# Kernel tuning notes

Measured on AMD Instinct MI355X. Metric: run time of the kernel, lower is better.

## Reference

```python
import jax, jax.numpy as jnp
import numpy as np

NUM_NODES = 50000
NUM_EDGES = 800000
NUM_GRAPHS = 1024
D_IN = 64
D_PROT = 1280
HID = 256
OUT = 1


def setup_inputs() -> dict:
    key = jax.random.key(0)
    ks = jax.random.split(key, 16)
    s = 0.02
    x = jax.random.normal(ks[0], (NUM_NODES, D_IN), dtype=jnp.float32)
    edge_index = jax.random.randint(ks[1], (2, NUM_EDGES), 0, NUM_NODES, dtype=jnp.int32)
    batch = jnp.sort(jax.random.randint(ks[2], (NUM_NODES,), 0, NUM_GRAPHS, dtype=jnp.int32))
    protein_embedding = jax.random.normal(ks[3], (NUM_GRAPHS, D_PROT), dtype=jnp.float32)
    # SAGEConv params: lin_l (aggregated neighbors, with bias), lin_r (self, no bias)
    Wl = jax.random.normal(ks[4], (D_IN, HID), dtype=jnp.float32) * s
    bl = jnp.zeros((HID,), dtype=jnp.float32)
    Wr = jax.random.normal(ks[5], (D_IN, HID), dtype=jnp.float32) * s
    Wp = jax.random.normal(ks[6], (D_PROT, HID), dtype=jnp.float32) * s
    bp = jnp.zeros((HID,), dtype=jnp.float32)
    Wi = jax.random.normal(ks[7], (2 * HID, HID), dtype=jnp.float32) * s
    bi = jnp.zeros((HID,), dtype=jnp.float32)
    Wo = jax.random.normal(ks[8], (HID, OUT), dtype=jnp.float32) * s
    bo = jnp.zeros((OUT,), dtype=jnp.float32)
    return {"x": x, "protein_embedding": protein_embedding, "Wl": Wl, "bl": bl,
            "Wr": Wr, "Wp": Wp, "bp": bp, "Wi": Wi, "bi": bi, "Wo": Wo, "bo": bo,
            "edge_index": edge_index, "batch": batch}


def _segment_mean(vals, seg_ids, num_segments):
    sums = jax.ops.segment_sum(vals, seg_ids, num_segments=num_segments)
    cnt = jax.ops.segment_sum(jnp.ones((vals.shape[0],), vals.dtype), seg_ids,
                              num_segments=num_segments)
    return sums / jnp.maximum(cnt, 1.0)[:, None]


def reference(x, protein_embedding, Wl, bl, Wr, Wp, bp, Wi, bi, Wo, bo, edge_index, batch):
    src, dst = edge_index[0], edge_index[1]
    # SAGEConv: mean-aggregate neighbor messages at target nodes, then fuse linears
    aggr = _segment_mean(x[src], dst, NUM_NODES)           # [N, D_IN]
    drug_x = jax.nn.relu(aggr @ Wl + bl + x @ Wr)          # [N, HID]
    # global_mean_pool over graphs in the batch
    pooled = _segment_mean(drug_x, batch, NUM_GRAPHS)      # [G, HID]
    protein_x = protein_embedding @ Wp + bp                # [G, HID]
    combined = jnp.concatenate((pooled, protein_x), axis=1)  # [G, 2*HID]
    interaction = jax.nn.relu(combined @ Wi + bi)          # [G, HID]
    return interaction @ Wo + bo                           # [G, OUT]
```

## Files before the change

### kernel.cpp

```cpp
#include <hip/hip_runtime.h>
#include <hip/hip_bf16.h>

#define N_NODES 50000
#define N_EDGES 800000
#define N_GRAPHS 1024
#define D_IN 64
#define D_PROT 1280
#define HID 256
#define N_PAD 50048

#define NB 782
#define BCAP 2048
#define BEPB 4096
#define BBLK 196

typedef __attribute__((ext_vector_type(8))) short short8;
typedef __attribute__((ext_vector_type(4))) float f32x4;
typedef __hip_bfloat16 bf16;

__device__ inline unsigned bf16rne(float f) {
  unsigned u = __float_as_uint(f);
  return (u + 0x7fffu + ((u >> 16) & 1u)) >> 16;
}
__device__ inline void acc_bf2(float4& a, uint2 v) {
  a.x += __uint_as_float(v.x << 16);
  a.y += __uint_as_float(v.x & 0xffff0000u);
  a.z += __uint_as_float(v.y << 16);
  a.w += __uint_as_float(v.y & 0xffff0000u);
}

#define PREP_XC 3125
#define PREP_PE (PREP_XC + 1280)
#define PREP_PL (PREP_PE + 8)
#define PREP_PR (PREP_PL + 8)
#define PREP_WP (PREP_PR + 160)
#define PREP_WI (PREP_WP + 64)

__device__ inline void pack_frag(const float* __restrict__ src, bf16* __restrict__ dst,
                                 int KC, int tid) {
  int lane = tid & 63;
  int chunk = tid >> 6;
  int c = chunk / KC, kc = chunk - c * KC;
  int kbase = kc * 32 + ((lane >> 4) * 8);
  int n = c * 16 + (lane & 15);
#pragma unroll
  for (int j = 0; j < 8; ++j)
    dst[(size_t)tid * 8 + j] = __float2bfloat16(src[(size_t)(kbase + j) * HID + n]);
}

__global__ __launch_bounds__(256) void k_front(
    const float* __restrict__ x, const float* __restrict__ pe,
    const float* __restrict__ Wl, const float* __restrict__ Wr,
    const float* __restrict__ Wp, const float* __restrict__ Wi,
    const int* __restrict__ ei,
    uint2* __restrict__ x2, uint2* __restrict__ pe2,
    bf16* __restrict__ Wl_pk, bf16* __restrict__ Wr_pk,
    bf16* __restrict__ Wp_pk, bf16* __restrict__ Wi_pk,
    int* __restrict__ bcnt, unsigned* __restrict__ bped) {
  __shared__ int hist[NB];
  __shared__ int base[NB];
  const int b = blockIdx.x;
  const int t = threadIdx.x;
  if (b < BBLK) {
    const int e0 = b * BEPB;
    for (int i = t; i < NB; i += 256) hist[i] = 0;
    __syncthreads();
    for (int i = t; i < BEPB; i += 1024) {
      int d[4]; bool v[4];
#pragma unroll
      for (int u = 0; u < 4; ++u) {
        int idx = i + u * 256;
        v[u] = (e0 + idx < N_EDGES);
        d[u] = v[u] ? ei[N_EDGES + e0 + idx] : 0;
      }
#pragma unroll
      for (int u = 0; u < 4; ++u)
        if (v[u]) atomicAdd(&hist[d[u] >> 6], 1);
    }
    __syncthreads();
    for (int i = t; i < NB; i += 256) {
      int c = hist[i];
      base[i] = (c > 0) ? atomicAdd(&bcnt[i], c) : 0;
      hist[i] = 0;
    }
    __syncthreads();
    for (int i = t; i < BEPB; i += 1024) {
      int s[4], d[4]; bool v[4];
#pragma unroll
      for (int u = 0; u < 4; ++u) {
        int idx = i + u * 256;
        v[u] = (e0 + idx < N_EDGES);
        s[u] = v[u] ? ei[e0 + idx] : 0;
        d[u] = v[u] ? ei[N_EDGES + e0 + idx] : 0;
      }
#pragma unroll
      for (int u = 0; u < 4; ++u) {
        if (v[u]) {
          int bk = d[u] >> 6;
          int pos = base[bk] + atomicAdd(&hist[bk], 1);
          if (pos < BCAP)
            bped[(size_t)bk * BCAP + pos] =
                (unsigned)s[u] | ((unsigned)(d[u] & 63) << 16);
        }
      }
    }
    return;
  }
  const int pb = b - BBLK;
  if (pb < PREP_XC) {
    int tid = pb * 256 + t;
    float4 v = ((const float4*)x)[tid];
    x2[tid] = make_uint2(bf16rne(v.x) | (bf16rne(v.y) << 16),
                         bf16rne(v.z) | (bf16rne(v.w) << 16));
  } else if (pb < PREP_PE) {
    int tid = (pb - PREP_XC) * 256 + t;
    float4 v = ((const float4*)pe)[tid];
    pe2[tid] = make_uint2(bf16rne(v.x) | (bf16rne(v.y) << 16),
                          bf16rne(v.z) | (bf16rne(v.w) << 16));
  } else if (pb < PREP_PL) {
    pack_frag(Wl, Wl_pk, 2, (pb - PREP_PE) * 256 + t);
  } else if (pb < PREP_PR) {
    pack_frag(Wr, Wr_pk, 2, (pb - PREP_PL) * 256 + t);
  } else if (pb < PREP_WP) {
    pack_frag(Wp, Wp_pk, 40, (pb - PREP_PR) * 256 + t);
  } else {
    pack_frag(Wi, Wi_pk, 16, (pb - PREP_WP) * 256 + t);
  }
}

__global__ __launch_bounds__(256, 4) void k_mid(
    const uint2* __restrict__ x2, const unsigned* __restrict__ bped,
    const int* __restrict__ bcnt, const int* __restrict__ batch,
    const bf16* __restrict__ Wl_pk, const bf16* __restrict__ Wr_pk,
    const float* __restrict__ bl, float* __restrict__ poolsum,
    const bf16* __restrict__ pebf, const bf16* __restrict__ Wp_pk,
    float* __restrict__ prot4) {
  __shared__ unsigned s_raw[2304];
  __shared__ unsigned short s_e[BCAP];
  __shared__ int s_off[65];
  __shared__ int s_cur[64];
  __shared__ int s_batch[64];
  const int t = threadIdx.x;
  if (blockIdx.x < NB) {
    uint2* aggT = (uint2*)s_raw;
    const int b = blockIdx.x;
    const int n0 = b * 64;
    const int nE = min(bcnt[b], BCAP);
    if (t < 64) s_cur[t] = 0;
    __syncthreads();
    for (int i = t; i < nE; i += 256) {
      unsigned pk = bped[(size_t)b * BCAP + i];
      s_raw[i] = pk;
      atomicAdd(&s_cur[(pk >> 16) & 63], 1);
    }
    __syncthreads();
    if (t < 64) {
      int sc = s_cur[t];
#pragma unroll
      for (int off = 1; off < 64; off <<= 1) {
        int u = __shfl_up(sc, off);
        if (t >= off) sc += u;
      }
      s_off[t + 1] = sc;
      if (t == 0) s_off[0] = 0;
      s_cur[t] = 0;
    }
    __syncthreads();
    for (int i = t; i < nE; i += 256) {
      unsigned pk = s_raw[i];
      int ld = (pk >> 16) & 63;
      int pos = s_off[ld] + atomicAdd(&s_cur[ld], 1);
      s_e[pos] = (unsigned short)(pk & 0xffffu);
    }
    if (t < 64) {
      int node = n0 + t;
      s_batch[t] = (node < N_NODES) ? batch[node] : 0x7fffffff;
    }
    __syncthreads();

    const int w = t >> 6, lane = t & 63;
    const int el = lane >> 4;
    const int fb = lane & 15;
    for (int n = w; n < 64; n += 4) {
      const int beg = s_off[n], end = s_off[n + 1];
      float4 s0 = {0,0,0,0}, s1 = {0,0,0,0}, s2 = {0,0,0,0}, s3 = {0,0,0,0};
      int e = beg;
      for (; e + 16 <= end; e += 16) {
        int i0 = s_e[e + el],     i1 = s_e[e + 4 + el];
        int i2 = s_e[e + 8 + el], i3 = s_e[e + 12 + el];
        uint2 v0 = x2[(size_t)i0 * 16 + fb];
        uint2 v1 = x2[(size_t)i1 * 16 + fb];
        uint2 v2 = x2[(size_t)i2 * 16 + fb];
        uint2 v3 = x2[(size_t)i3 * 16 + fb];
        acc_bf2(s0, v0); acc_bf2(s1, v1); acc_bf2(s2, v2); acc_bf2(s3, v3);
      }
      for (; e + 4 <= end; e += 4)
        acc_bf2(s0, x2[(size_t)s_e[e + el] * 16 + fb]);
      if (e + el < end)
        acc_bf2(s1, x2[(size_t)s_e[e + el] * 16 + fb]);
      float4 tt;
      tt.x = (s0.x + s1.x) + (s2.x + s3.x);
      tt.y = (s0.y + s1.y) + (s2.y + s3.y);
      tt.z = (s0.z + s1.z) + (s2.z + s3.z);
      tt.w = (s0.w + s1.w) + (s2.w + s3.w);
      tt.x += __shfl_xor(tt.x, 32); tt.x += __shfl_xor(tt.x, 16);
      tt.y += __shfl_xor(tt.y, 32); tt.y += __shfl_xor(tt.y, 16);
      tt.z += __shfl_xor(tt.z, 32); tt.z += __shfl_xor(tt.z, 16);
      tt.w += __shfl_xor(tt.w, 32); tt.w += __shfl_xor(tt.w, 16);
      if (el == 0) {
        float inv = 1.0f / (float)max(end - beg, 1);
        uint2 o;
        o.x = bf16rne(tt.x * inv) | (bf16rne(tt.y * inv) << 16);
        o.y = bf16rne(tt.z * inv) | (bf16rne(tt.w * inv) << 16);
        aggT[n * 18 + fb] = o;
      }
    }
    __syncthreads();

    const int ml = lane & 15, q = lane >> 4;
    const int lv = min(63, N_NODES - 1 - n0);
    float bic[4];
#pragma unroll
    for (int cl = 0; cl < 4; ++cl) bic[cl] = bl[w * 64 + cl * 16 + ml];
#pragma unroll
    for (int rt = 0; rt < 4; ++rt) {
      f32x4 acc[4];
#pragma unroll
      for (int cl = 0; cl < 4; ++cl) acc[cl] = (f32x4){0.f, 0.f, 0.f, 0.f};
      const int arow = rt * 16 + ml;
#pragma unroll
      for (int kc = 0; kc < 2; ++kc) {
        short8 a0 = *(const short8*)(&aggT[arow * 18 + kc * 8 + q * 2]);
#pragma unroll
        for (int cl = 0; cl < 4; ++cl) {
          short8 bb = *(const short8*)(Wl_pk + ((size_t)((w * 4 + cl) * 2 + kc) * 64 + lane) * 8);
          acc[cl] = __builtin_amdgcn_mfma_f32_16x16x32_bf16(a0, bb, acc[cl], 0, 0, 0);
        }
        short8 a1 = *(const short8*)((const bf16*)x2 + (size_t)(n0 + arow) * D_IN + kc * 32 + q * 8);
#pragma unroll
        for (int cl = 0; cl < 4; ++cl) {
          short8 bb = *(const short8*)(Wr_pk + ((size_t)((w * 4 + cl) * 2 + kc) * 64 + lane) * 8);
          acc[cl] = __builtin_amdgcn_mfma_f32_16x16x32_bf16(a1, bb, acc[cl], 0, 0, 0);
        }
      }
      float vv[4][4];
      int bt[4];
#pragma unroll
      for (int i = 0; i < 4; ++i) bt[i] = s_batch[rt * 16 + q * 4 + i];
#pragma unroll
      for (int cl = 0; cl < 4; ++cl)
#pragma unroll
        for (int i = 0; i < 4; ++i)
          vv[cl][i] = fmaxf(acc[cl][i] + bic[cl], 0.f);
      const int glo = s_batch[min(rt * 16, lv)];
      const int ghi = s_batch[min(rt * 16 + 15, lv)];
      for (int g = glo; g <= ghi; ++g) {
#pragma unroll
        for (int cl = 0; cl < 4; ++cl) {
          float s = 0.f;
#pragma unroll
          for (int i = 0; i < 4; ++i) s += (bt[i] == g) ? vv[cl][i] : 0.f;
          s += __shfl_xor(s, 16); s += __shfl_xor(s, 32);
          if (q == 0)
            atomicAdd(&poolsum[(size_t)g * HID + (w * 64 + cl * 16 + ml)], s);
        }
      }
    }
    return;
  }
  const int kb = blockIdx.x - NB;
  const int w = t >> 6, lane = t & 63;
  const int ml = lane & 15, q = lane >> 4;
  const int mt = kb >> 2, ks = kb & 3;
  const int g0 = mt * 16, kc0 = ks * 10;
  f32x4 acc[4];
#pragma unroll
  for (int c = 0; c < 4; ++c) acc[c] = (f32x4){0.f, 0.f, 0.f, 0.f};
  for (int kc = kc0; kc < kc0 + 10; ++kc) {
    short8 a = *(const short8*)(pebf + (size_t)(g0 + ml) * D_PROT + kc * 32 + q * 8);
#pragma unroll
    for (int cl = 0; cl < 4; ++cl) {
      short8 bb = *(const short8*)(Wp_pk + ((size_t)((w * 4 + cl) * 40 + kc) * 64 + lane) * 8);
      acc[cl] = __builtin_amdgcn_mfma_f32_16x16x32_bf16(a, bb, acc[cl], 0, 0, 0);
    }
  }
#pragma unroll
  for (int cl = 0; cl < 4; ++cl) {
    const int col = w * 64 + cl * 16 + ml;
#pragma unroll
    for (int i = 0; i < 4; ++i)
      prot4[((size_t)ks * N_GRAPHS + g0 + q * 4 + i) * HID + col] = acc[cl][i];
  }
}

__device__ inline int lb_dev(const int* __restrict__ a, int v) {
  int lo = 0, hi = N_NODES;
  while (lo < hi) { int m = (lo + hi) >> 1; if (a[m] < v) lo = m + 1; else hi = m; }
  return lo;
}

__global__ __launch_bounds__(256) void k_tail(
    const float* __restrict__ poolsum, const int* __restrict__ batch,
    const float* __restrict__ prot4, const float* __restrict__ bp,
    const bf16* __restrict__ Wi_pk, const float* __restrict__ bi,
    const float* __restrict__ Wo, const float* __restrict__ bo,
    float* __restrict__ out) {
  __shared__ bf16 aT[16][520];
  __shared__ float s_inv[16];
  __shared__ float sRed[16 * 4];
  const int t = threadIdx.x, w = t >> 6, lane = t & 63;
  const int ml = lane & 15, q = lane >> 4;
  const int g0 = blockIdx.x * 16;
  if (t < 16) {
    int lo = lb_dev(batch, g0 + t), hi = lb_dev(batch, g0 + t + 1);
    s_inv[t] = 1.0f / (float)max(hi - lo, 1);
  }
  __syncthreads();
  for (int idx = t; idx < 16 * 512; idx += 256) {
    const int row = idx >> 9, col = idx & 511;
    float v;
    if (col < HID) {
      v = poolsum[(size_t)(g0 + row) * HID + col] * s_inv[row];
    } else {
      const int c = col - HID;
      const size_t base = (size_t)(g0 + row) * HID + c;
      v = prot4[base] + prot4[(size_t)N_GRAPHS * HID + base]
        + prot4[2 * (size_t)N_GRAPHS * HID + base]
        + prot4[3 * (size_t)N_GRAPHS * HID + base] + bp[c];
    }
    aT[row][col] = __float2bfloat16(v);
  }
  __syncthreads();
  f32x4 acc[4];
#pragma unroll
  for (int c = 0; c < 4; ++c) acc[c] = (f32x4){0.f, 0.f, 0.f, 0.f};
  for (int kc = 0; kc < 16; ++kc) {
    short8 a = *(const short8*)(&aT[ml][kc * 32 + q * 8]);
#pragma unroll
    for (int cl = 0; cl < 4; ++cl) {
      short8 bb = *(const short8*)(Wi_pk + ((size_t)((w * 4 + cl) * 16 + kc) * 64 + lane) * 8);
      acc[cl] = __builtin_amdgcn_mfma_f32_16x16x32_bf16(a, bb, acc[cl], 0, 0, 0);
    }
  }
  float bic[4], woc[4];
#pragma unroll
  for (int cl = 0; cl < 4; ++cl) {
    const int col = w * 64 + cl * 16 + ml;
    bic[cl] = bi[col];
    woc[cl] = Wo[col];
  }
#pragma unroll
  for (int i = 0; i < 4; ++i) {
    float s = 0.f;
#pragma unroll
    for (int cl = 0; cl < 4; ++cl)
      s += fmaxf(acc[cl][i] + bic[cl], 0.f) * woc[cl];
    s += __shfl_xor(s, 1); s += __shfl_xor(s, 2);
    s += __shfl_xor(s, 4); s += __shfl_xor(s, 8);
    if (ml == 0) sRed[(q * 4 + i) * 4 + w] = s;
  }
  __syncthreads();
  if (t < 16)
    out[g0 + t] = sRed[t * 4 + 0] + sRed[t * 4 + 1] + sRed[t * 4 + 2]
                + sRed[t * 4 + 3] + bo[0];
}

extern "C" void kernel_launch(void* const* d_in, const int* in_sizes, int n_in,
                              void* d_out, int out_size, void* d_ws, size_t ws_size,
                              hipStream_t stream) {
  const float* x     = (const float*)d_in[0];
  const float* pe    = (const float*)d_in[1];
  const float* Wl    = (const float*)d_in[2];
  const float* bl    = (const float*)d_in[3];
  const float* Wr    = (const float*)d_in[4];
  const float* Wp    = (const float*)d_in[5];
  const float* bp    = (const float*)d_in[6];
  const float* Wi    = (const float*)d_in[7];
  const float* bi    = (const float*)d_in[8];
  const float* Wo    = (const float*)d_in[9];
  const float* bo    = (const float*)d_in[10];
  const int*   ei    = (const int*)d_in[11];
  const int*   batch = (const int*)d_in[12];
  float* out = (float*)d_out;

  char* p = (char*)d_ws;
  auto alloc = [&](size_t bytes) {
    char* r = p;
    p += (bytes + 255) & ~(size_t)255;
    return r;
  };
  int*   bcnt    = (int*)alloc(NB * 4);
  float* poolsum = (float*)alloc((size_t)N_GRAPHS * HID * 4);
  size_t zbytes = (size_t)(p - (char*)d_ws);
  unsigned* bped  = (unsigned*)alloc((size_t)NB * BCAP * 4);
  bf16*  xbf    = (bf16*)alloc((size_t)N_PAD * D_IN * 2);
  bf16*  pebf   = (bf16*)alloc((size_t)N_GRAPHS * D_PROT * 2);
  bf16*  Wl_pk  = (bf16*)alloc((size_t)D_IN * HID * 2);
  bf16*  Wr_pk  = (bf16*)alloc((size_t)D_IN * HID * 2);
  bf16*  Wp_pk  = (bf16*)alloc((size_t)D_PROT * HID * 2);
  bf16*  Wi_pk  = (bf16*)alloc((size_t)2 * HID * HID * 2);
  float* prot4  = (float*)alloc((size_t)4 * N_GRAPHS * HID * 4);

  (void)hipMemsetAsync(d_ws, 0, zbytes, stream);

  k_front<<<BBLK + PREP_WI, 256, 0, stream>>>(
      x, pe, Wl, Wr, Wp, Wi, ei,
      (uint2*)xbf, (uint2*)pebf, Wl_pk, Wr_pk, Wp_pk, Wi_pk, bcnt, bped);
  k_mid<<<NB + 256, 256, 0, stream>>>(
      (const uint2*)xbf, bped, bcnt, batch, Wl_pk, Wr_pk, bl, poolsum,
      pebf, Wp_pk, prot4);
  k_tail<<<N_GRAPHS / 16, 256, 0, stream>>>(
      poolsum, batch, prot4, bp, Wi_pk, bi, Wo, bo, out);
}
```

Before: 167.4 us.

## Drop split-K for protein GEMM, emit bf16 with bias; halve edge-bin block size

The protein projection no longer splits K four ways into fp32 partials. Each of 64 blocks now runs the full K=1280 loop, adds the bias and writes bf16 directly, so the tail kernel reads one small bf16 buffer instead of summing four fp32 partials. The edge-binning front kernel also uses twice as many blocks, each handling half as many edges. The aim is less partial-sum traffic and a simpler tail, at the cost of fewer, longer-running protein GEMM blocks running alongside the aggregation blocks.

```diff
diff --git a/kernel.cpp b/kernel.cpp
--- a/kernel.cpp
+++ b/kernel.cpp
@@ -11,8 +11,8 @@
 
 #define NB 782
 #define BCAP 2048
-#define BEPB 4096
-#define BBLK 196
+#define BEPB 2048
+#define BBLK 391
 
 typedef __attribute__((ext_vector_type(8))) short short8;
 typedef __attribute__((ext_vector_type(4))) float f32x4;
@@ -134,7 +134,7 @@
     const bf16* __restrict__ Wl_pk, const bf16* __restrict__ Wr_pk,
     const float* __restrict__ bl, float* __restrict__ poolsum,
     const bf16* __restrict__ pebf, const bf16* __restrict__ Wp_pk,
-    float* __restrict__ prot4) {
+    const float* __restrict__ bp, unsigned short* __restrict__ protC) {
   __shared__ unsigned s_raw[2304];
   __shared__ unsigned short s_e[BCAP];
   __shared__ int s_off[65];
@@ -271,12 +271,11 @@
   const int kb = blockIdx.x - NB;
   const int w = t >> 6, lane = t & 63;
   const int ml = lane & 15, q = lane >> 4;
-  const int mt = kb >> 2, ks = kb & 3;
-  const int g0 = mt * 16, kc0 = ks * 10;
+  const int g0 = kb * 16;
   f32x4 acc[4];
 #pragma unroll
   for (int c = 0; c < 4; ++c) acc[c] = (f32x4){0.f, 0.f, 0.f, 0.f};
-  for (int kc = kc0; kc < kc0 + 10; ++kc) {
+  for (int kc = 0; kc < 40; ++kc) {
     short8 a = *(const short8*)(pebf + (size_t)(g0 + ml) * D_PROT + kc * 32 + q * 8);
 #pragma unroll
     for (int cl = 0; cl < 4; ++cl) {
@@ -287,9 +286,11 @@
 #pragma unroll
   for (int cl = 0; cl < 4; ++cl) {
     const int col = w * 64 + cl * 16 + ml;
+    const float bpc = bp[col];
 #pragma unroll
     for (int i = 0; i < 4; ++i)
-      prot4[((size_t)ks * N_GRAPHS + g0 + q * 4 + i) * HID + col] = acc[cl][i];
+      protC[(size_t)(g0 + q * 4 + i) * HID + col] =
+          (unsigned short)bf16rne(acc[cl][i] + bpc);
   }
 }
 
@@ -301,7 +302,7 @@
 
 __global__ __launch_bounds__(256) void k_tail(
     const float* __restrict__ poolsum, const int* __restrict__ batch,
-    const float* __restrict__ prot4, const float* __restrict__ bp,
+    const unsigned short* __restrict__ protC,
     const bf16* __restrict__ Wi_pk, const float* __restrict__ bi,
     const float* __restrict__ Wo, const float* __restrict__ bo,
     float* __restrict__ out) {
@@ -316,19 +317,12 @@
     s_inv[t] = 1.0f / (float)max(hi - lo, 1);
   }
   __syncthreads();
-  for (int idx = t; idx < 16 * 512; idx += 256) {
-    const int row = idx >> 9, col = idx & 511;
-    float v;
-    if (col < HID) {
-      v = poolsum[(size_t)(g0 + row) * HID + col] * s_inv[row];
-    } else {
-      const int c = col - HID;
-      const size_t base = (size_t)(g0 + row) * HID + c;
-      v = prot4[base] + prot4[(size_t)N_GRAPHS * HID + base]
-        + prot4[2 * (size_t)N_GRAPHS * HID + base]
-        + prot4[3 * (size_t)N_GRAPHS * HID + base] + bp[c];
-    }
-    aT[row][col] = __float2bfloat16(v);
+  for (int idx = t; idx < 16 * 256; idx += 256) {
+    const int row = idx >> 8, col = idx & 255;
+    float v = poolsum[(size_t)(g0 + row) * HID + col] * s_inv[row];
+    ((unsigned short*)&aT[row][0])[col] = (unsigned short)bf16rne(v);
+    ((unsigned short*)&aT[row][0])[HID + col] =
+        protC[(size_t)(g0 + row) * HID + col];
   }
   __syncthreads();
   f32x4 acc[4];
@@ -399,16 +393,16 @@
   bf16*  Wr_pk  = (bf16*)alloc((size_t)D_IN * HID * 2);
   bf16*  Wp_pk  = (bf16*)alloc((size_t)D_PROT * HID * 2);
   bf16*  Wi_pk  = (bf16*)alloc((size_t)2 * HID * HID * 2);
-  float* prot4  = (float*)alloc((size_t)4 * N_GRAPHS * HID * 4);
+  unsigned short* protC = (unsigned short*)alloc((size_t)N_GRAPHS * HID * 2);
 
   (void)hipMemsetAsync(d_ws, 0, zbytes, stream);
 
   k_front<<<BBLK + PREP_WI, 256, 0, stream>>>(
       x, pe, Wl, Wr, Wp, Wi, ei,
       (uint2*)xbf, (uint2*)pebf, Wl_pk, Wr_pk, Wp_pk, Wi_pk, bcnt, bped);
-  k_mid<<<NB + 256, 256, 0, stream>>>(
+  k_mid<<<NB + 64, 256, 0, stream>>>(
       (const uint2*)xbf, bped, bcnt, batch, Wl_pk, Wr_pk, bl, poolsum,
-      pebf, Wp_pk, prot4);
+      pebf, Wp_pk, bp, protC);
   k_tail<<<N_GRAPHS / 16, 256, 0, stream>>>(
-      poolsum, batch, prot4, bp, Wi_pk, bi, Wo, bo, out);
-}
+      poolsum, batch, protC, Wi_pk, bi, Wo, bo, out);
+}
```

Result: faster. 157.6 us (-5.9%).
